# Kernel tuning notes

Hardware: AMD Instinct MI355X
Metric: run time of the kernel (lower is better)

The kernel has to match this reference:

```python
import jax, jax.numpy as jnp
import numpy as np

KH, KW = 3, 3
STRIDE = 1
PADDING = 1
CIN, COUT = 64, 64


def setup_inputs() -> dict:
    key = jax.random.key(0)
    kx, kw, kb = jax.random.split(key, 3)
    x = jax.random.normal(kx, (16, CIN, 112, 112), dtype=jnp.float32)
    # Kaiming-uniform style init, matching the torch module
    fan = CIN * KH * KW
    gain = np.sqrt(2.0)
    bound_w = np.sqrt(3.0) * gain / np.sqrt(fan)
    weights = jax.random.uniform(kw, (COUT, CIN, KH, KW), dtype=jnp.float32,
                                 minval=-bound_w, maxval=bound_w)
    bound_b = 1.0 / np.sqrt(fan)
    bias = jax.random.uniform(kb, (COUT,), dtype=jnp.float32,
                              minval=-bound_b, maxval=bound_b)
    return {"x": x, "weights": weights, "bias": bias}


def reference(x, weights, bias):
    # Equivalent to F.unfold + GEMM: a standard cross-correlation conv.
    # x: (N, C, H, W), weights: (F, C, KH, KW) -> out: (N, F, H', W')
    out = jax.lax.conv_general_dilated(
        x, weights,
        window_strides=(STRIDE, STRIDE),
        padding=((PADDING, PADDING), (PADDING, PADDING)),
        dimension_numbers=("NCHW", "OIHW", "NCHW"),
    )
    return out + bias[None, :, None, None]
```

## Files before the change

### kernel.cpp

```cpp
#include <hip/hip_runtime.h>


typedef __attribute__((ext_vector_type(8))) short bf16x8;
typedef __attribute__((ext_vector_type(4))) float f32x4;

#define CIN 64
#define COUT 64
#define HH 112
#define WW 112

#define XP 72
#define WCOLS 114
#define LDS_SHORTS (3 * WCOLS * XP)
#define OP 113

__device__ __forceinline__ unsigned short f2bf(float f) {
    unsigned u = __builtin_bit_cast(unsigned, f);
    u += 0x7FFFu + ((u >> 16) & 1u);
    return (unsigned short)(u >> 16);
}

__global__ void conv_wprep(const float* __restrict__ w, short* __restrict__ wbf) {
    int i = blockIdx.x * 256 + threadIdx.x;
    int j = i & 7;
    int f = (i >> 3) & 63;
    int koct = (i >> 9) & 3;
    int cb = (i >> 11) & 1;
    int t = i >> 12;
    int c = cb * 32 + koct * 8 + j;
    int ky = t / 3, kx = t - ky * 3;
    wbf[i] = (short)f2bf(w[((f * CIN + c) * 3 + ky) * 3 + kx]);
}

__global__ __launch_bounds__(256, 3)
void conv3x3_mfma(const float* __restrict__ x, const short* __restrict__ wbf,
                  const float* __restrict__ bias, float* __restrict__ out)
{
    __shared__ __align__(16) short lds[LDS_SHORTS];
    const int tid = threadIdx.x;
    const int n = blockIdx.x;
    const int h = blockIdx.y;

    const int wave = tid >> 6;
    const int lane = tid & 63;
    const int lm = lane & 15;
    const int q  = lane >> 4;

    const short* wlane = wbf + (q * 512 + (wave * 16 + lm) * 8);
    bf16x8 bfr[9][2];
#pragma unroll
    for (int t = 0; t < 9; ++t) {
        bfr[t][0] = *(const bf16x8*)(wlane + t * 4096);
        bfr[t][1] = *(const bf16x8*)(wlane + t * 4096 + 2048);
    }

    if (tid < 96) {
        int e = tid & 15;
        int g = tid >> 4;
        int dy = g >> 1;
        int wcol = (g & 1) ? (WCOLS - 1) : 0;
        *(uint2*)&lds[((dy * WCOLS + wcol) * 36 + e * 2) * 2] = (uint2){0u, 0u};
    }
    if (h == 0) {
        for (int i = tid; i < WCOLS * 16; i += 256) {
            int wcol = i >> 4, e = i & 15;
            *(uint2*)&lds[((0 * WCOLS + wcol) * 36 + e * 2) * 2] = (uint2){0u, 0u};
        }
    }
    if (h == HH - 1) {
        for (int i = tid; i < WCOLS * 16; i += 256) {
            int wcol = i >> 4, e = i & 15;
            *(uint2*)&lds[((2 * WCOLS + wcol) * 36 + e * 2) * 2] = (uint2){0u, 0u};
        }
    }
    for (int i = tid; i < 3 * 16 * 28; i += 256) {
        int w4 = i % 28;
        int rp = i / 28;
        int dy = rp >> 4;
        int cq = rp & 15;
        int gh = h + dy - 1;
        if ((unsigned)gh < (unsigned)HH) {
            int c = cq * 4;
            const float* px = x + (((n * CIN + c) * HH + gh) * WW + w4 * 4);
            const float4 v0 = *(const float4*)px;
            const float4 v1 = *(const float4*)(px + HH * WW);
            const float4 v2 = *(const float4*)(px + 2 * HH * WW);
            const float4 v3 = *(const float4*)(px + 3 * HH * WW);
            int o = cq >> 1, p = cq & 1;
            float a0[4] = {v0.x, v0.y, v0.z, v0.w};
            float a1[4] = {v1.x, v1.y, v1.z, v1.w};
            float a2[4] = {v2.x, v2.y, v2.z, v2.w};
            float a3[4] = {v3.x, v3.y, v3.z, v3.w};
#pragma unroll
            for (int dw = 0; dw < 4; ++dw) {
                int wcol = 1 + w4 * 4 + dw;
                int swz = (wcol >> 2) & 7;
                int dslot = 4 * (o ^ swz) + 2 * p;
                uint2 pk;
                pk.x = (unsigned)f2bf(a0[dw]) | ((unsigned)f2bf(a1[dw]) << 16);
                pk.y = (unsigned)f2bf(a2[dw]) | ((unsigned)f2bf(a3[dw]) << 16);
                *(uint2*)&lds[((dy * WCOLS + wcol) * 36 + dslot) * 2] = pk;
            }
        }
    }
    __syncthreads();

    f32x4 acc[7];
#pragma unroll
    for (int mt = 0; mt < 7; ++mt) acc[mt] = (f32x4){0.f, 0.f, 0.f, 0.f};

#pragma unroll
    for (int ky = 0; ky < 3; ++ky) {
#pragma unroll
        for (int kx = 0; kx < 3; ++kx) {
            const int t = ky * 3 + kx;
#pragma unroll
            for (int mt = 0; mt < 7; ++mt) {
                int wcol = mt * 16 + lm + kx;
                int swz = (wcol >> 2) & 7;
                int base = (ky * WCOLS + wcol) * XP;
                bf16x8 a0 = *(const bf16x8*)&lds[base + 8 * (q ^ swz)];
                bf16x8 a1 = *(const bf16x8*)&lds[base + 8 * ((q + 4) ^ swz)];
                acc[mt] = __builtin_amdgcn_mfma_f32_16x16x32_bf16(a0, bfr[t][0], acc[mt], 0, 0, 0);
                acc[mt] = __builtin_amdgcn_mfma_f32_16x16x32_bf16(a1, bfr[t][1], acc[mt], 0, 0, 0);
            }
        }
    }

    __syncthreads();
    float* lout = (float*)lds;
#pragma unroll
    for (int mt = 0; mt < 7; ++mt) {
#pragma unroll
        for (int r = 0; r < 4; ++r) {
            int p = mt * 16 + (q << 2) + r;
            lout[(wave * 16 + lm) * OP + p] = acc[mt][r];
        }
    }
    __syncthreads();
    for (int i = tid; i < 64 * 28; i += 256) {
        int f = i / 28;
        int w4 = i - f * 28;
        float b = bias[f];
        const float* lp = lout + f * OP + w4 * 4;
        float4 v;
        v.x = lp[0] + b; v.y = lp[1] + b; v.z = lp[2] + b; v.w = lp[3] + b;
        *(float4*)(out + (((n * COUT + f) * HH + h) * WW + w4 * 4)) = v;
    }
}

extern "C" void kernel_launch(void* const* d_in, const int* in_sizes, int n_in,
                              void* d_out, int out_size, void* d_ws, size_t ws_size,
                              hipStream_t stream) {
    const float* x = (const float*)d_in[0];
    const float* w = (const float*)d_in[1];
    const float* b = (const float*)d_in[2];
    float* out = (float*)d_out;
    short* wbf = (short*)d_ws;

    conv_wprep<<<144, 256, 0, stream>>>(w, wbf);
    dim3 grid(16, HH);
    conv3x3_mfma<<<grid, 256, 0, stream>>>(x, wbf, b, out);
}
```

Measured before the change: 125.3 us.

## Compute four output rows per block with waves split by row over all filters

Each block now covers four output rows instead of one. It stages six input rows in LDS, so the halo rows are shared across the rows of the tile. Work is split across waves by output row rather than by filter group, so each wave computes all 64 filters with a 7x4 accumulator tile. Weight fragments are double-buffered from global memory per tap. The epilogue writes in two passes through LDS. This cuts redundant input loads and conversions but raises register pressure, drops occupancy to one block, and shrinks the grid to 448 blocks.

```diff
diff --git a/kernel.cpp b/kernel.cpp
--- a/kernel.cpp
+++ b/kernel.cpp
@@ -8,11 +8,12 @@
 #define COUT 64
 #define HH 112
 #define WW 112
+#define ROWS 4
+#define DYS  6
 
 #define XP 72
 #define WCOLS 114
-#define LDS_SHORTS (3 * WCOLS * XP)
-#define OP 113
+#define LDS_SHORTS (DYS * WCOLS * XP)
 
 __device__ __forceinline__ unsigned short f2bf(float f) {
     unsigned u = __builtin_bit_cast(unsigned, f);
@@ -32,53 +33,45 @@
     wbf[i] = (short)f2bf(w[((f * CIN + c) * 3 + ky) * 3 + kx]);
 }
 
-__global__ __launch_bounds__(256, 3)
+__global__ __launch_bounds__(256, 1)
 void conv3x3_mfma(const float* __restrict__ x, const short* __restrict__ wbf,
                   const float* __restrict__ bias, float* __restrict__ out)
 {
     __shared__ __align__(16) short lds[LDS_SHORTS];
     const int tid = threadIdx.x;
     const int n = blockIdx.x;
-    const int h = blockIdx.y;
+    const int h0 = blockIdx.y * ROWS;
 
     const int wave = tid >> 6;
     const int lane = tid & 63;
     const int lm = lane & 15;
     const int q  = lane >> 4;
 
-    const short* wlane = wbf + (q * 512 + (wave * 16 + lm) * 8);
-    bf16x8 bfr[9][2];
-#pragma unroll
-    for (int t = 0; t < 9; ++t) {
-        bfr[t][0] = *(const bf16x8*)(wlane + t * 4096);
-        bfr[t][1] = *(const bf16x8*)(wlane + t * 4096 + 2048);
-    }
-
-    if (tid < 96) {
+    if (tid < 192) {
         int e = tid & 15;
         int g = tid >> 4;
         int dy = g >> 1;
         int wcol = (g & 1) ? (WCOLS - 1) : 0;
         *(uint2*)&lds[((dy * WCOLS + wcol) * 36 + e * 2) * 2] = (uint2){0u, 0u};
     }
-    if (h == 0) {
+    if (h0 == 0) {
         for (int i = tid; i < WCOLS * 16; i += 256) {
             int wcol = i >> 4, e = i & 15;
             *(uint2*)&lds[((0 * WCOLS + wcol) * 36 + e * 2) * 2] = (uint2){0u, 0u};
         }
     }
-    if (h == HH - 1) {
+    if (h0 == HH - ROWS) {
         for (int i = tid; i < WCOLS * 16; i += 256) {
             int wcol = i >> 4, e = i & 15;
-            *(uint2*)&lds[((2 * WCOLS + wcol) * 36 + e * 2) * 2] = (uint2){0u, 0u};
+            *(uint2*)&lds[((5 * WCOLS + wcol) * 36 + e * 2) * 2] = (uint2){0u, 0u};
         }
     }
-    for (int i = tid; i < 3 * 16 * 28; i += 256) {
+    for (int i = tid; i < DYS * 16 * 28; i += 256) {
         int w4 = i % 28;
         int rp = i / 28;
         int dy = rp >> 4;
         int cq = rp & 15;
-        int gh = h + dy - 1;
+        int gh = h0 + dy - 1;
         if ((unsigned)gh < (unsigned)HH) {
             int c = cq * 4;
             const float* px = x + (((n * CIN + c) * HH + gh) * WW + w4 * 4);
@@ -103,49 +96,74 @@
             }
         }
     }
+
+    bf16x8 br[2][4][2];
+#pragma unroll
+    for (int nt = 0; nt < 4; ++nt) {
+        br[0][nt][0] = *(const bf16x8*)(wbf + (0 * 8 + q) * 512 + (nt * 16 + lm) * 8);
+        br[0][nt][1] = *(const bf16x8*)(wbf + (0 * 8 + 4 + q) * 512 + (nt * 16 + lm) * 8);
+    }
+
     __syncthreads();
 
-    f32x4 acc[7];
+    f32x4 acc[7][4];
 #pragma unroll
-    for (int mt = 0; mt < 7; ++mt) acc[mt] = (f32x4){0.f, 0.f, 0.f, 0.f};
+    for (int mt = 0; mt < 7; ++mt)
+#pragma unroll
+        for (int nt = 0; nt < 4; ++nt) acc[mt][nt] = (f32x4){0.f, 0.f, 0.f, 0.f};
 
 #pragma unroll
-    for (int ky = 0; ky < 3; ++ky) {
+    for (int t = 0; t < 9; ++t) {
+        const int buf = t & 1;
+        if (t < 8) {
 #pragma unroll
-        for (int kx = 0; kx < 3; ++kx) {
-            const int t = ky * 3 + kx;
+            for (int nt = 0; nt < 4; ++nt) {
+                br[1 - buf][nt][0] = *(const bf16x8*)(wbf + ((t + 1) * 8 + q) * 512 + (nt * 16 + lm) * 8);
+                br[1 - buf][nt][1] = *(const bf16x8*)(wbf + ((t + 1) * 8 + 4 + q) * 512 + (nt * 16 + lm) * 8);
+            }
+        }
+        const int ky = t / 3, kx = t - ky * 3;
 #pragma unroll
-            for (int mt = 0; mt < 7; ++mt) {
-                int wcol = mt * 16 + lm + kx;
-                int swz = (wcol >> 2) & 7;
-                int base = (ky * WCOLS + wcol) * XP;
-                bf16x8 a0 = *(const bf16x8*)&lds[base + 8 * (q ^ swz)];
-                bf16x8 a1 = *(const bf16x8*)&lds[base + 8 * ((q + 4) ^ swz)];
-                acc[mt] = __builtin_amdgcn_mfma_f32_16x16x32_bf16(a0, bfr[t][0], acc[mt], 0, 0, 0);
-                acc[mt] = __builtin_amdgcn_mfma_f32_16x16x32_bf16(a1, bfr[t][1], acc[mt], 0, 0, 0);
-            }
+        for (int mt = 0; mt < 7; ++mt) {
+            int wcol = mt * 16 + lm + kx;
+            int swz = (wcol >> 2) & 7;
+            int base = ((wave + ky) * WCOLS + wcol) * XP;
+            bf16x8 a0 = *(const bf16x8*)&lds[base + 8 * (q ^ swz)];
+            bf16x8 a1 = *(const bf16x8*)&lds[base + 8 * ((q + 4) ^ swz)];
+#pragma unroll
+            for (int nt = 0; nt < 4; ++nt)
+                acc[mt][nt] = __builtin_amdgcn_mfma_f32_16x16x32_bf16(a0, br[buf][nt][0], acc[mt][nt], 0, 0, 0);
+#pragma unroll
+            for (int nt = 0; nt < 4; ++nt)
+                acc[mt][nt] = __builtin_amdgcn_mfma_f32_16x16x32_bf16(a1, br[buf][nt][1], acc[mt][nt], 0, 0, 0);
         }
     }
 
-    __syncthreads();
     float* lout = (float*)lds;
 #pragma unroll
-    for (int mt = 0; mt < 7; ++mt) {
+    for (int pass = 0; pass < 2; ++pass) {
+        __syncthreads();
 #pragma unroll
-        for (int r = 0; r < 4; ++r) {
-            int p = mt * 16 + (q << 2) + r;
-            lout[(wave * 16 + lm) * OP + p] = acc[mt][r];
+        for (int mt = 0; mt < 7; ++mt)
+#pragma unroll
+            for (int ntl = 0; ntl < 2; ++ntl) {
+                const f32x4 v = acc[mt][pass * 2 + ntl];
+#pragma unroll
+                for (int r = 0; r < 4; ++r)
+                    lout[(wave * 32 + ntl * 16 + lm) * 113 + mt * 16 + q * 4 + r] = v[r];
+            }
+        __syncthreads();
+        for (int i = tid; i < 128 * 28; i += 256) {
+            int fr = i / 28;
+            int w4 = i - fr * 28;
+            int w = fr >> 5;
+            int f = pass * 32 + (fr & 31);
+            float b = bias[f];
+            const float* lp = lout + fr * 113 + w4 * 4;
+            float4 v;
+            v.x = lp[0] + b; v.y = lp[1] + b; v.z = lp[2] + b; v.w = lp[3] + b;
+            *(float4*)(out + (((n * COUT + f) * HH + h0 + w) * WW + w4 * 4)) = v;
         }
-    }
-    __syncthreads();
-    for (int i = tid; i < 64 * 28; i += 256) {
-        int f = i / 28;
-        int w4 = i - f * 28;
-        float b = bias[f];
-        const float* lp = lout + f * OP + w4 * 4;
-        float4 v;
-        v.x = lp[0] + b; v.y = lp[1] + b; v.z = lp[2] + b; v.w = lp[3] + b;
-        *(float4*)(out + (((n * COUT + f) * HH + h) * WW + w4 * 4)) = v;
     }
 }
 
@@ -159,6 +177,6 @@
     short* wbf = (short*)d_ws;
 
     conv_wprep<<<144, 256, 0, stream>>>(w, wbf);
-    dim3 grid(16, HH);
+    dim3 grid(16, HH / ROWS);
     conv3x3_mfma<<<grid, 256, 0, stream>>>(x, wbf, b, out);
 }
```

After: 130.1 us. 1.04x slower.

## Pre-transform input to padded NHWC bf16 and run single-wave MFMA conv from global

Applied to the files above, without the earlier changes.

Adds a separate pass that converts the fp32 NCHW input into a zero-padded NHWC bf16 buffer in workspace. The conv kernel then becomes a one-wave block that loads A fragments straight from global or cache and holds all 64 output channels in registers (7x4 accumulators), looping over 18 K-slices. This removes the redundant per-block LDS staging and conversion of three input rows, and the LDS transpose epilogue. The cost is an extra kernel launch and a round trip of the converted input through memory, plus uncoalesced-ish direct global loads and high register pressure.

```diff
diff --git a/kernel.cpp b/kernel.cpp
--- a/kernel.cpp
+++ b/kernel.cpp
@@ -8,17 +8,26 @@
 #define COUT 64
 #define HH 112
 #define WW 112
-
-#define XP 72
-#define WCOLS 114
-#define LDS_SHORTS (3 * WCOLS * XP)
-#define OP 113
+#define XTW 114
+#define WBF_BYTES 73728
 
 __device__ __forceinline__ unsigned short f2bf(float f) {
     unsigned u = __builtin_bit_cast(unsigned, f);
     u += 0x7FFFu + ((u >> 16) & 1u);
     return (unsigned short)(u >> 16);
 }
+
+#if __has_builtin(__builtin_amdgcn_cvt_pk_bf16_f32)
+__device__ __forceinline__ unsigned pk2bf(float a, float b) {
+    typedef __attribute__((ext_vector_type(2))) __bf16 bf16x2;
+    bf16x2 r = __builtin_amdgcn_cvt_pk_bf16_f32(a, b);
+    return __builtin_bit_cast(unsigned, r);
+}
+#else
+__device__ __forceinline__ unsigned pk2bf(float a, float b) {
+    return (unsigned)f2bf(a) | ((unsigned)f2bf(b) << 16);
+}
+#endif
 
 __global__ void conv_wprep(const float* __restrict__ w, short* __restrict__ wbf) {
     int i = blockIdx.x * 256 + threadIdx.x;
@@ -32,120 +41,120 @@
     wbf[i] = (short)f2bf(w[((f * CIN + c) * 3 + ky) * 3 + kx]);
 }
 
-__global__ __launch_bounds__(256, 3)
-void conv3x3_mfma(const float* __restrict__ x, const short* __restrict__ wbf,
-                  const float* __restrict__ bias, float* __restrict__ out)
+__global__ __launch_bounds__(256)
+void conv_xform(const float* __restrict__ x, short* __restrict__ xt) {
+    const int n = blockIdx.x;
+    const int hp = blockIdx.y;
+    const int tid = threadIdx.x;
+    short* dst = xt + ((size_t)(n * XTW + hp) * XTW) * 64;
+
+    if (hp == 0 || hp == XTW - 1) {
+        for (int i = tid; i < XTW * 16; i += 256)
+            *(uint2*)(dst + i * 4) = (uint2){0u, 0u};
+        return;
+    }
+
+    __shared__ short lrow[WW * 66];
+    const int h = hp - 1;
+    for (int u = tid; u < 448; u += 256) {
+        int w4 = u % 28;
+        int cq = u / 28;
+        int c = cq * 4;
+        const float* px = x + (((size_t)(n * CIN + c) * HH + h) * WW) + w4 * 4;
+        const float4 v0 = *(const float4*)px;
+        const float4 v1 = *(const float4*)(px + HH * WW);
+        const float4 v2 = *(const float4*)(px + 2 * HH * WW);
+        const float4 v3 = *(const float4*)(px + 3 * HH * WW);
+        float a0[4] = {v0.x, v0.y, v0.z, v0.w};
+        float a1[4] = {v1.x, v1.y, v1.z, v1.w};
+        float a2[4] = {v2.x, v2.y, v2.z, v2.w};
+        float a3[4] = {v3.x, v3.y, v3.z, v3.w};
+#pragma unroll
+        for (int dw = 0; dw < 4; ++dw) {
+            int w = w4 * 4 + dw;
+            *(unsigned*)&lrow[w * 66 + c]     = pk2bf(a0[dw], a1[dw]);
+            *(unsigned*)&lrow[w * 66 + c + 2] = pk2bf(a2[dw], a3[dw]);
+        }
+    }
+    __syncthreads();
+    for (int u = tid; u < 1824; u += 256) {
+        uint2 val;
+        int wp, s;
+        if (u < 1792) {
+            int p = u >> 4;
+            s = u & 15;
+            val.x = *(const unsigned*)&lrow[p * 66 + s * 4];
+            val.y = *(const unsigned*)&lrow[p * 66 + s * 4 + 2];
+            wp = p + 1;
+        } else {
+            int b = u - 1792;
+            wp = (b >> 4) ? (XTW - 1) : 0;
+            s = b & 15;
+            val = (uint2){0u, 0u};
+        }
+        *(uint2*)(dst + wp * 64 + s * 4) = val;
+    }
+}
+
+__global__ __launch_bounds__(64, 2)
+void conv_mfma(const short* __restrict__ xt, const short* __restrict__ wbf,
+               const float* __restrict__ bias, float* __restrict__ out)
 {
-    __shared__ __align__(16) short lds[LDS_SHORTS];
-    const int tid = threadIdx.x;
     const int n = blockIdx.x;
     const int h = blockIdx.y;
-
-    const int wave = tid >> 6;
-    const int lane = tid & 63;
+    const int lane = threadIdx.x;
     const int lm = lane & 15;
     const int q  = lane >> 4;
 
-    const short* wlane = wbf + (q * 512 + (wave * 16 + lm) * 8);
-    bf16x8 bfr[9][2];
+    float bsr[4];
 #pragma unroll
-    for (int t = 0; t < 9; ++t) {
-        bfr[t][0] = *(const bf16x8*)(wlane + t * 4096);
-        bfr[t][1] = *(const bf16x8*)(wlane + t * 4096 + 2048);
+    for (int ntl = 0; ntl < 4; ++ntl) bsr[ntl] = bias[ntl * 16 + lm];
+
+    const short* arow = xt + ((size_t)(n * XTW + h) * XTW + lm) * 64 + q * 8;
+    const short* wl = wbf + q * 512 + lm * 8;
+
+    f32x4 acc[7][4];
+#pragma unroll
+    for (int mt = 0; mt < 7; ++mt)
+#pragma unroll
+        for (int ntl = 0; ntl < 4; ++ntl) acc[mt][ntl] = (f32x4){0.f, 0.f, 0.f, 0.f};
+
+#pragma unroll 1
+    for (int ht = 0; ht < 18; ++ht) {
+        const int t = ht >> 1, cb = ht & 1;
+        const int ky = t / 3, kx = t - ky * 3;
+
+        const short* ab = arow + (ky * XTW + kx) * 64 + cb * 32;
+        bf16x8 a[7];
+#pragma unroll
+        for (int mt = 0; mt < 7; ++mt)
+            a[mt] = *(const bf16x8*)(ab + mt * 1024);
+
+        const short* wn = wl + (t * 8 + cb * 4) * 512;
+        bf16x8 Bf[4];
+#pragma unroll
+        for (int ntl = 0; ntl < 4; ++ntl)
+            Bf[ntl] = *(const bf16x8*)(wn + ntl * 128);
+
+#pragma unroll
+        for (int mt = 0; mt < 7; ++mt)
+#pragma unroll
+            for (int ntl = 0; ntl < 4; ++ntl)
+                acc[mt][ntl] = __builtin_amdgcn_mfma_f32_16x16x32_bf16(
+                    a[mt], Bf[ntl], acc[mt][ntl], 0, 0, 0);
     }
 
-    if (tid < 96) {
-        int e = tid & 15;
-        int g = tid >> 4;
-        int dy = g >> 1;
-        int wcol = (g & 1) ? (WCOLS - 1) : 0;
-        *(uint2*)&lds[((dy * WCOLS + wcol) * 36 + e * 2) * 2] = (uint2){0u, 0u};
-    }
-    if (h == 0) {
-        for (int i = tid; i < WCOLS * 16; i += 256) {
-            int wcol = i >> 4, e = i & 15;
-            *(uint2*)&lds[((0 * WCOLS + wcol) * 36 + e * 2) * 2] = (uint2){0u, 0u};
+#pragma unroll
+    for (int ntl = 0; ntl < 4; ++ntl) {
+        float* ob = out + (((size_t)(n * COUT + ntl * 16 + lm) * HH + h) * WW) + q * 4;
+        const float b = bsr[ntl];
+#pragma unroll
+        for (int mt = 0; mt < 7; ++mt) {
+            const f32x4 v = acc[mt][ntl];
+            float4 s;
+            s.x = v[0] + b; s.y = v[1] + b; s.z = v[2] + b; s.w = v[3] + b;
+            *(float4*)(ob + mt * 16) = s;
         }
-    }
-    if (h == HH - 1) {
-        for (int i = tid; i < WCOLS * 16; i += 256) {
-            int wcol = i >> 4, e = i & 15;
-            *(uint2*)&lds[((2 * WCOLS + wcol) * 36 + e * 2) * 2] = (uint2){0u, 0u};
-        }
-    }
-    for (int i = tid; i < 3 * 16 * 28; i += 256) {
-        int w4 = i % 28;
-        int rp = i / 28;
-        int dy = rp >> 4;
-        int cq = rp & 15;
-        int gh = h + dy - 1;
-        if ((unsigned)gh < (unsigned)HH) {
-            int c = cq * 4;
-            const float* px = x + (((n * CIN + c) * HH + gh) * WW + w4 * 4);
-            const float4 v0 = *(const float4*)px;
-            const float4 v1 = *(const float4*)(px + HH * WW);
-            const float4 v2 = *(const float4*)(px + 2 * HH * WW);
-            const float4 v3 = *(const float4*)(px + 3 * HH * WW);
-            int o = cq >> 1, p = cq & 1;
-            float a0[4] = {v0.x, v0.y, v0.z, v0.w};
-            float a1[4] = {v1.x, v1.y, v1.z, v1.w};
-            float a2[4] = {v2.x, v2.y, v2.z, v2.w};
-            float a3[4] = {v3.x, v3.y, v3.z, v3.w};
-#pragma unroll
-            for (int dw = 0; dw < 4; ++dw) {
-                int wcol = 1 + w4 * 4 + dw;
-                int swz = (wcol >> 2) & 7;
-                int dslot = 4 * (o ^ swz) + 2 * p;
-                uint2 pk;
-                pk.x = (unsigned)f2bf(a0[dw]) | ((unsigned)f2bf(a1[dw]) << 16);
-                pk.y = (unsigned)f2bf(a2[dw]) | ((unsigned)f2bf(a3[dw]) << 16);
-                *(uint2*)&lds[((dy * WCOLS + wcol) * 36 + dslot) * 2] = pk;
-            }
-        }
-    }
-    __syncthreads();
-
-    f32x4 acc[7];
-#pragma unroll
-    for (int mt = 0; mt < 7; ++mt) acc[mt] = (f32x4){0.f, 0.f, 0.f, 0.f};
-
-#pragma unroll
-    for (int ky = 0; ky < 3; ++ky) {
-#pragma unroll
-        for (int kx = 0; kx < 3; ++kx) {
-            const int t = ky * 3 + kx;
-#pragma unroll
-            for (int mt = 0; mt < 7; ++mt) {
-                int wcol = mt * 16 + lm + kx;
-                int swz = (wcol >> 2) & 7;
-                int base = (ky * WCOLS + wcol) * XP;
-                bf16x8 a0 = *(const bf16x8*)&lds[base + 8 * (q ^ swz)];
-                bf16x8 a1 = *(const bf16x8*)&lds[base + 8 * ((q + 4) ^ swz)];
-                acc[mt] = __builtin_amdgcn_mfma_f32_16x16x32_bf16(a0, bfr[t][0], acc[mt], 0, 0, 0);
-                acc[mt] = __builtin_amdgcn_mfma_f32_16x16x32_bf16(a1, bfr[t][1], acc[mt], 0, 0, 0);
-            }
-        }
-    }
-
-    __syncthreads();
-    float* lout = (float*)lds;
-#pragma unroll
-    for (int mt = 0; mt < 7; ++mt) {
-#pragma unroll
-        for (int r = 0; r < 4; ++r) {
-            int p = mt * 16 + (q << 2) + r;
-            lout[(wave * 16 + lm) * OP + p] = acc[mt][r];
-        }
-    }
-    __syncthreads();
-    for (int i = tid; i < 64 * 28; i += 256) {
-        int f = i / 28;
-        int w4 = i - f * 28;
-        float b = bias[f];
-        const float* lp = lout + f * OP + w4 * 4;
-        float4 v;
-        v.x = lp[0] + b; v.y = lp[1] + b; v.z = lp[2] + b; v.w = lp[3] + b;
-        *(float4*)(out + (((n * COUT + f) * HH + h) * WW + w4 * 4)) = v;
     }
 }
 
@@ -157,8 +166,9 @@
     const float* b = (const float*)d_in[2];
     float* out = (float*)d_out;
     short* wbf = (short*)d_ws;
+    short* xt  = (short*)((char*)d_ws + WBF_BYTES);
 
     conv_wprep<<<144, 256, 0, stream>>>(w, wbf);
-    dim3 grid(16, HH);
-    conv3x3_mfma<<<grid, 256, 0, stream>>>(x, wbf, b, out);
+    conv_xform<<<dim3(16, XTW), 256, 0, stream>>>(x, xt);
+    conv_mfma<<<dim3(16, HH), 64, 0, stream>>>(xt, wbf, b, out);
 }
```

Result: slower. 143.4 us (+14.5%).
